# Kernel optimization log

Hardware: AMD Instinct MI355X
Metric: run time of the kernel (lower is better)

## Reference

```python
import math
import jax, jax.numpy as jnp
import numpy as np

CLUSTER_RATIO1 = 0.0625
CLUSTER_RATIO2 = 0.35
K_LAYER1 = 8
K_LAYER2 = 3


def _dpc_knn(x, cluster_num, k, key):
    """Density-peak clustering with KNN density. x: [B,N,C] -> idx_cluster [B,N]."""
    B, N, C = x.shape
    sq = jnp.sum(x * x, axis=-1)  # [B,N]
    d2 = sq[:, :, None] + sq[:, None, :] - 2.0 * jnp.einsum('bnc,bmc->bnm', x, x)
    dist = jnp.sqrt(jnp.maximum(d2, 0.0)) / jnp.sqrt(jnp.asarray(C, x.dtype))  # cdist / C**0.5
    # k nearest (smallest) distances
    neg_dn, _ = jax.lax.top_k(-dist, k)
    dist_nearest = -neg_dn  # [B,N,k]
    density = jnp.exp(-jnp.mean(dist_nearest ** 2, axis=-1))
    density = density + jax.random.uniform(key, density.shape, dtype=density.dtype) * 1e-6
    mask = (density[:, None, :] > density[:, :, None]).astype(x.dtype)  # [B,N,N]
    dist_max = jnp.max(dist.reshape(B, -1), axis=-1)[:, None, None]
    parent_dist = jnp.min(dist * mask + dist_max * (1.0 - mask), axis=-1)  # [B,N]
    score = parent_dist * density
    _, index_down = jax.lax.top_k(score, cluster_num)  # [B,cluster_num] cluster centers
    # assign each token to nearest center
    dm = jnp.take_along_axis(dist, index_down[:, :, None], axis=1)  # [B,cluster_num,N]
    idx_cluster = jnp.argmin(dm, axis=1)  # [B,N]
    bidx = jnp.arange(B)[:, None]
    idx_cluster = idx_cluster.at[bidx, index_down].set(
        jnp.broadcast_to(jnp.arange(cluster_num)[None, :], index_down.shape))
    return idx_cluster


def _merge_tokens(x, idx_cluster, cluster_num):
    """Weighted (uniform) scatter-mean of tokens into clusters. x: [B,N,C]."""
    B, N, C = x.shape
    flat = (idx_cluster + jnp.arange(B)[:, None] * cluster_num).reshape(-1)  # [B*N]
    ones = jnp.ones((B * N,), x.dtype)
    all_w = jax.ops.segment_sum(ones, flat, num_segments=B * cluster_num) + 1e-6
    norm_w = 1.0 / all_w[flat]  # token_weight == 1
    merged = jax.ops.segment_sum(x.reshape(B * N, C) * norm_w[:, None], flat,
                                 num_segments=B * cluster_num)
    return merged.reshape(B, cluster_num, C)


def _group(meta1, meta2, idx_cluster2, score_w, score_b):
    """Reorder [meta2[v]; members of cluster v from meta1] per cluster, scaled by modulation."""
    T, K1, C = meta1.shape
    K2 = meta2.shape[1]
    modu = jax.nn.softmax(meta2.mean(axis=2) @ score_w.T + score_b, axis=-1)  # [T,K2]
    # composite sort key: (cluster_id, 0 for meta2 center, 1+i for meta1 member i) -> stable grouping
    cid = jnp.concatenate([jnp.broadcast_to(jnp.arange(K2)[None, :], (T, K2)),
                           idx_cluster2], axis=1)  # [T,K2+K1]
    pos = jnp.concatenate([jnp.zeros((T, K2), jnp.int32),
                           jnp.broadcast_to(jnp.arange(1, K1 + 1, dtype=jnp.int32)[None, :], (T, K1))],
                          axis=1)
    sort_key = cid * (K1 + 2) + pos
    order = jnp.argsort(sort_key, axis=1)  # stable; keys are unique anyway
    tokens = jnp.concatenate([meta2, meta1], axis=1)  # [T,K2+K1,C]
    sorted_tokens = jnp.take_along_axis(tokens, order[:, :, None], axis=1)
    sorted_cid = jnp.take_along_axis(cid, order, axis=1)
    scale = jnp.take_along_axis(modu, sorted_cid, axis=1)  # [T,K2+K1]
    return sorted_tokens * scale[:, :, None]


def setup_inputs() -> dict:
    key = jax.random.key(0)
    k1, k2, k3 = jax.random.split(key, 3)
    T, N, C = 128, 256, 1408
    vis_embed = jax.random.normal(k1, (T, N, C), dtype=jnp.float32)
    score_w = jax.random.normal(k2, (6, 6), dtype=jnp.float32) * 0.1
    score_b = jax.random.normal(k3, (6,), dtype=jnp.float32) * 0.1
    return {"vis_embed": vis_embed, "score_w": score_w, "score_b": score_b}


def reference(vis_embed, score_w, score_b):
    T, N, C = vis_embed.shape
    cn1 = max(math.ceil(N * CLUSTER_RATIO1), 1)      # 16
    cn2 = max(math.ceil(cn1 * CLUSTER_RATIO2), 1)    # 6
    nk = jax.random.split(jax.random.key(42), 2)
    idx1 = _dpc_knn(vis_embed, cn1, K_LAYER1, nk[0])
    meta1 = _merge_tokens(vis_embed, idx1, cn1)       # [T,16,C]
    idx2 = _dpc_knn(meta1, cn2, K_LAYER2, nk[1])
    meta2 = _merge_tokens(meta1, idx2, cn2)           # [T,6,C]
    return _group(meta1, meta2, idx2, score_w, score_b)  # [T,22,C]
```

## Files before the change

kernel.cpp:

```cpp
#include <hip/hip_runtime.h>
#include <math.h>

#define T_BATCH 128
#define N_TOK   256
#define C_DIM   1408
#define CN1     16
#define KNN1    8
#define CN2     6
#define KNN2    3
#define NOUT    22
#define LS      44

typedef __attribute__((ext_vector_type(4))) short sh4;
typedef __attribute__((ext_vector_type(8))) short sh8;
typedef __attribute__((ext_vector_type(4))) float f32x4;
typedef __fp16 h2v __attribute__((ext_vector_type(2)));
typedef __fp16 h8v __attribute__((ext_vector_type(8)));

union frag_u { sh4 h[2]; sh8 v; };
union h8u { sh8 s; h8v h; };
union h2u { h2v h; unsigned u; };

__device__ inline h8v ld_frag(const short* p) {
    frag_u u;
    u.h[0] = *(const sh4*)p;
    u.h[1] = *(const sh4*)(p + 4);
    h8u o; o.s = u.v;
    return o.h;
}

__device__ inline void split2(float v0, float v1, unsigned& hip, unsigned& lop) {
    h2v h = __builtin_amdgcn_cvt_pkrtz(v0, v1);
    float r0 = v0 - (float)h[0];
    float r1 = v1 - (float)h[1];
    h2v l = __builtin_amdgcn_cvt_pkrtz(r0, r1);
    h2u uh, ul;
    uh.h = h; ul.h = l;
    hip = uh.u;
    lop = ul.u;
}

#define INS8(m, v) {                                   \
    float _x = (v);                                    \
    _Pragma("unroll")                                  \
    for (int _q = 0; _q < 8; _q++) {                   \
        float _lo = fminf(m[_q], _x);                  \
        _x = fmaxf(m[_q], _x);                         \
        m[_q] = _lo;                                   \
    }                                                  \
}

__global__ __launch_bounds__(256, 4) void gemm_dist_sym(const float* __restrict__ x,
                                                        float* __restrict__ dist) {
    const int id = blockIdx.x;
    const int r  = id & 7;
    const int q8 = id >> 3;
    const int p  = q8 % 10;
    const int tt = q8 / 10;
    const int t  = tt * 8 + r;
    const int bi = (p < 4) ? 0 : (p < 7) ? 1 : (p < 9) ? 2 : 3;
    const int bj = (p < 4) ? p : (p < 7) ? p - 3 : (p < 9) ? p - 5 : 3;
    const int i0 = bi * 64, j0 = bj * 64;
    const bool diag = (bi == bj);
    const float* X = x + (size_t)t * N_TOK * C_DIM;

    __shared__ short Ahi[64 * LS], Alo[64 * LS], Bhi[64 * LS], Blo[64 * LS];
    __shared__ float nred[512];
    __shared__ float snA[64], snB[64];

    const int tid  = threadIdx.x;
    const int wave = tid >> 6;
    const int lane = tid & 63;
    const int qr   = wave >> 1;
    const int qc   = wave & 1;
    const int srow = tid >> 2;
    const int sq   = tid & 3;
    const int fr   = lane & 15;
    const int fq   = lane >> 4;

    const short* BhiS = diag ? Ahi : Bhi;
    const short* BloS = diag ? Alo : Blo;

    f32x4 acc[2][2];
#pragma unroll
    for (int a = 0; a < 2; a++)
#pragma unroll
        for (int b = 0; b < 2; b++) acc[a][b] = (f32x4){0.f, 0.f, 0.f, 0.f};

    const float* Arow = X + (size_t)(i0 + srow) * C_DIM + sq * 8;
    const float* Brow = X + (size_t)(j0 + srow) * C_DIM + sq * 8;
    float nA = 0.f, nB = 0.f;

    float4 a0 = *(const float4*)(Arow + 0);
    float4 a1 = *(const float4*)(Arow + 4);
    float4 b0 = {0.f, 0.f, 0.f, 0.f}, b1 = {0.f, 0.f, 0.f, 0.f};
    if (!diag) {
        b0 = *(const float4*)(Brow + 0);
        b1 = *(const float4*)(Brow + 4);
    }

    for (int k0 = 0; k0 < C_DIM; k0 += 32) {
        float av[8], bv[8];
        av[0] = a0.x; av[1] = a0.y; av[2] = a0.z; av[3] = a0.w;
        av[4] = a1.x; av[5] = a1.y; av[6] = a1.z; av[7] = a1.w;
#pragma unroll
        for (int e = 0; e < 8; e++) nA += av[e] * av[e];
        unsigned ah[4], al[4], bh[4], bl[4];
#pragma unroll
        for (int q = 0; q < 4; q++) split2(av[2 * q], av[2 * q + 1], ah[q], al[q]);
        if (!diag) {
            bv[0] = b0.x; bv[1] = b0.y; bv[2] = b0.z; bv[3] = b0.w;
            bv[4] = b1.x; bv[5] = b1.y; bv[6] = b1.z; bv[7] = b1.w;
#pragma unroll
            for (int e = 0; e < 8; e++) nB += bv[e] * bv[e];
#pragma unroll
            for (int q = 0; q < 4; q++) split2(bv[2 * q], bv[2 * q + 1], bh[q], bl[q]);
        }
        __syncthreads();
        {
            unsigned* AH = (unsigned*)&Ahi[srow * LS + sq * 8];
            unsigned* AL = (unsigned*)&Alo[srow * LS + sq * 8];
#pragma unroll
            for (int q = 0; q < 4; q++) { AH[q] = ah[q]; AL[q] = al[q]; }
            if (!diag) {
                unsigned* BH = (unsigned*)&Bhi[srow * LS + sq * 8];
                unsigned* BL = (unsigned*)&Blo[srow * LS + sq * 8];
#pragma unroll
                for (int q = 0; q < 4; q++) { BH[q] = bh[q]; BL[q] = bl[q]; }
            }
        }
        __syncthreads();

        const int k1 = k0 + 32;
        if (k1 < C_DIM) {
            a0 = *(const float4*)(Arow + k1);
            a1 = *(const float4*)(Arow + k1 + 4);
            if (!diag) {
                b0 = *(const float4*)(Brow + k1);
                b1 = *(const float4*)(Brow + k1 + 4);
            }
        }

        h8v fAh[2], fAl[2], fBh[2], fBl[2];
#pragma unroll
        for (int mt = 0; mt < 2; mt++) {
            int ro = (qr * 32 + mt * 16 + fr) * LS + fq * 8;
            fAh[mt] = ld_frag(&Ahi[ro]);
            fAl[mt] = ld_frag(&Alo[ro]);
            int co = (qc * 32 + mt * 16 + fr) * LS + fq * 8;
            fBh[mt] = ld_frag(&BhiS[co]);
            fBl[mt] = ld_frag(&BloS[co]);
        }
#pragma unroll
        for (int mt = 0; mt < 2; mt++)
#pragma unroll
            for (int nt = 0; nt < 2; nt++) {
                acc[mt][nt] = __builtin_amdgcn_mfma_f32_16x16x32_f16(fAh[mt], fBh[nt], acc[mt][nt], 0, 0, 0);
                acc[mt][nt] = __builtin_amdgcn_mfma_f32_16x16x32_f16(fAh[mt], fBl[nt], acc[mt][nt], 0, 0, 0);
                acc[mt][nt] = __builtin_amdgcn_mfma_f32_16x16x32_f16(fAl[mt], fBh[nt], acc[mt][nt], 0, 0, 0);
            }
    }

    nred[tid] = nA;
    nred[256 + tid] = diag ? nA : nB;
    __syncthreads();
    if (tid < 64) {
        snA[tid] = nred[4 * tid] + nred[4 * tid + 1] + nred[4 * tid + 2] + nred[4 * tid + 3];
        snB[tid] = nred[256 + 4 * tid] + nred[256 + 4 * tid + 1]
                 + nred[256 + 4 * tid + 2] + nred[256 + 4 * tid + 3];
    }
    __syncthreads();

    const float inv_sqrtC = 1.0f / sqrtf((float)C_DIM);
    float* Dt = dist + (size_t)t * N_TOK * N_TOK;
#pragma unroll
    for (int mt = 0; mt < 2; mt++)
#pragma unroll
        for (int nt = 0; nt < 2; nt++) {
            int jl = qc * 32 + nt * 16 + fr;
            int jg = j0 + jl;
            float sqj = snB[jl];
            int il0 = qr * 32 + mt * 16 + fq * 4;
            float vv[4];
#pragma unroll
            for (int rr = 0; rr < 4; rr++) {
                int ig = i0 + il0 + rr;
                float d2 = snA[il0 + rr] + sqj - 2.0f * acc[mt][nt][rr];
                float v = (ig == jg) ? 0.0f : sqrtf(fmaxf(d2, 0.0f)) * inv_sqrtC;
                Dt[(size_t)ig * N_TOK + jg] = v;
                vv[rr] = v;
            }
            if (!diag) {
                float4 o; o.x = vv[0]; o.y = vv[1]; o.z = vv[2]; o.w = vv[3];
                *(float4*)&Dt[(size_t)jg * N_TOK + i0 + il0] = o;
            }
        }
}

__global__ __launch_bounds__(1024) void dpc1_fused(const float* __restrict__ dist,
                                                   int* __restrict__ memb,
                                                   int* __restrict__ cntg,
                                                   int* __restrict__ offg) {
    const int t    = blockIdx.x;
    const int tid  = threadIdx.x;
    const int col  = tid & 255;
    const int h    = tid >> 8;
    const int lane = tid & 63;
    const int wid  = tid >> 6;
    const float* D = dist + (size_t)t * N_TOK * N_TOK;

    __shared__ float dens_s[N_TOK];
    __shared__ float lists[KNN1][1024];
    __shared__ float red[1024];
    __shared__ float rmax16[16];
    __shared__ unsigned long long wred[16];
    __shared__ int centers[CN1];
    __shared__ int bks[N_TOK];
    __shared__ int cnt_s[CN1], off_s[CN1];

    float c0[8], c1[8];
#pragma unroll
    for (int q = 0; q < 8; q++) { c0[q] = 3.4e38f; c1[q] = 3.4e38f; }
    float mx = 0.f;
    const float* base = D + (size_t)(h * 64) * N_TOK + col;
    for (int jj = 0; jj < 64; jj += 2) {
        float d0 = base[(size_t)(jj + 0) * N_TOK];
        float d1 = base[(size_t)(jj + 1) * N_TOK];
        mx = fmaxf(mx, fmaxf(d0, d1));
        INS8(c0, d0); INS8(c1, d1);
    }
#pragma unroll
    for (int q = 0; q < 8; q++) { INS8(c0, c1[q]); }
#pragma unroll
    for (int q = 0; q < 8; q++) lists[q][tid] = c0[q];
#pragma unroll
    for (int off = 32; off > 0; off >>= 1) mx = fmaxf(mx, __shfl_xor(mx, off));
    if (lane == 0) rmax16[wid] = mx;
    __syncthreads();
    float dmax = rmax16[0];
#pragma unroll
    for (int w = 1; w < 16; w++) dmax = fmaxf(dmax, rmax16[w]);

    if (h == 0) {
#pragma unroll
        for (int s = 1; s < 4; s++)
#pragma unroll
            for (int q = 0; q < 8; q++) { float v = lists[q][col + s * 256]; INS8(c0, v); }
        float s2 = 0.f;
#pragma unroll
        for (int q = 0; q < 8; q++) s2 += c0[q] * c0[q];
        dens_s[col] = expf(-s2 / (float)KNN1);
    }
    __syncthreads();
    const float dens = dens_s[col];

    float p0 = dmax, p1 = dmax;
    const float* dsh = dens_s + h * 64;
    for (int jj = 0; jj < 64; jj += 2) {
        float d0 = base[(size_t)(jj + 0) * N_TOK];
        float d1 = base[(size_t)(jj + 1) * N_TOK];
        p0 = (dsh[jj + 0] > dens) ? fminf(p0, d0) : p0;
        p1 = (dsh[jj + 1] > dens) ? fminf(p1, d1) : p1;
    }
    red[tid] = fminf(p0, p1);
    __syncthreads();
    float score = 0.f;
    if (h == 0)
        score = fminf(fminf(red[col], red[col + 256]),
                      fminf(red[col + 512], red[col + 768])) * dens;

    unsigned long long key = 0;
    if (h == 0)
        key = ((unsigned long long)__float_as_uint(score) << 32) | (unsigned)(65535 - col);
    for (int k = 0; k < CN1; k++) {
        unsigned long long mm = key;
#pragma unroll
        for (int off = 32; off > 0; off >>= 1) {
            unsigned long long o = __shfl_xor(mm, off);
            mm = (o > mm) ? o : mm;
        }
        if (lane == 0) wred[wid] = mm;
        __syncthreads();
        unsigned long long b = wred[0];
#pragma unroll
        for (int w = 1; w < 16; w++) b = (wred[w] > b) ? wred[w] : b;
        int idx = 65535 - (int)(b & 0xFFFFull);
        if (tid == 0) centers[k] = idx;
        if (tid == idx) key = 0;
        __syncthreads();
    }

    int bk = 0;
    if (h == 0) {
        float bd = 3.4e38f;
#pragma unroll
        for (int k = 0; k < CN1; k++) {
            float d = D[(size_t)centers[k] * N_TOK + col];
            if (d < bd) { bd = d; bk = k; }
        }
#pragma unroll
        for (int k = 0; k < CN1; k++) if (col == centers[k]) bk = k;
        bks[col] = bk;
    }
    __syncthreads();
    if (tid < CN1) {
        int c = 0;
        for (int j = 0; j < N_TOK; j++) c += (bks[j] == tid);
        cnt_s[tid] = c;
    }
    __syncthreads();
    if (tid == 0) {
        int o = 0;
        for (int q = 0; q < CN1; q++) { off_s[q] = o; o += cnt_s[q]; }
    }
    __syncthreads();
    if (h == 0) {
        int rank = 0;
        for (int j = 0; j < col; j++) rank += (bks[j] == bk);
        memb[t * N_TOK + off_s[bk] + rank] = col;
    }
    if (tid < CN1) {
        cntg[t * CN1 + tid] = cnt_s[tid];
        offg[t * CN1 + tid] = off_s[tid];
    }
}

__global__ __launch_bounds__(256) void merge1_kernel(const float* __restrict__ x,
                                                     const int* __restrict__ memb,
                                                     const int* __restrict__ cntg,
                                                     const int* __restrict__ offg,
                                                     float* __restrict__ meta1) {
    const int q   = blockIdx.x;
    const int t   = blockIdx.y;
    const int tid = threadIdx.x;
    const int n    = cntg[t * CN1 + q];
    const int base = t * N_TOK + offg[t * CN1 + q];
    const int c0 = tid, c1 = tid + 256;
    const bool act1 = (c1 < C_DIM / 4);
    const float4* xb = (const float4*)(x + (size_t)t * N_TOK * C_DIM);
    const int stride4 = C_DIM / 4;

    float4 s0 = {0.f, 0.f, 0.f, 0.f};
    float4 s1 = {0.f, 0.f, 0.f, 0.f};
    int m = 0;
    for (; m + 4 <= n; m += 4) {
        int r0 = memb[base + m + 0];
        int r1 = memb[base + m + 1];
        int r2 = memb[base + m + 2];
        int r3 = memb[base + m + 3];
        float4 a0 = xb[(size_t)r0 * stride4 + c0];
        float4 a1 = xb[(size_t)r1 * stride4 + c0];
        float4 a2 = xb[(size_t)r2 * stride4 + c0];
        float4 a3 = xb[(size_t)r3 * stride4 + c0];
        s0.x += a0.x; s0.y += a0.y; s0.z += a0.z; s0.w += a0.w;
        s0.x += a1.x; s0.y += a1.y; s0.z += a1.z; s0.w += a1.w;
        s0.x += a2.x; s0.y += a2.y; s0.z += a2.z; s0.w += a2.w;
        s0.x += a3.x; s0.y += a3.y; s0.z += a3.z; s0.w += a3.w;
        if (act1) {
            float4 b0 = xb[(size_t)r0 * stride4 + c1];
            float4 b1 = xb[(size_t)r1 * stride4 + c1];
            float4 b2 = xb[(size_t)r2 * stride4 + c1];
            float4 b3 = xb[(size_t)r3 * stride4 + c1];
            s1.x += b0.x; s1.y += b0.y; s1.z += b0.z; s1.w += b0.w;
            s1.x += b1.x; s1.y += b1.y; s1.z += b1.z; s1.w += b1.w;
            s1.x += b2.x; s1.y += b2.y; s1.z += b2.z; s1.w += b2.w;
            s1.x += b3.x; s1.y += b3.y; s1.z += b3.z; s1.w += b3.w;
        }
    }
    for (; m < n; m++) {
        int r0 = memb[base + m];
        float4 a0 = xb[(size_t)r0 * stride4 + c0];
        s0.x += a0.x; s0.y += a0.y; s0.z += a0.z; s0.w += a0.w;
        if (act1) {
            float4 b0 = xb[(size_t)r0 * stride4 + c1];
            s1.x += b0.x; s1.y += b0.y; s1.z += b0.z; s1.w += b0.w;
        }
    }
    float w = 1.0f / ((float)n + 1e-6f);
    float4* mr = (float4*)(meta1 + ((size_t)t * CN1 + q) * C_DIM);
    float4 o0; o0.x = s0.x * w; o0.y = s0.y * w; o0.z = s0.z * w; o0.w = s0.w * w;
    mr[c0] = o0;
    if (act1) {
        float4 o1; o1.x = s1.x * w; o1.y = s1.y * w; o1.z = s1.z * w; o1.w = s1.w * w;
        mr[c1] = o1;
    }
}

__global__ __launch_bounds__(1024) void layer2_kernel(const float* __restrict__ meta1,
                                                      const float* __restrict__ score_w,
                                                      const float* __restrict__ score_b,
                                                      float* __restrict__ out) {
    const int t   = blockIdx.x & 127;
    const int bh  = blockIdx.x >> 7;
    const int tid = threadIdx.x;
    const float* M = meta1 + (size_t)t * CN1 * C_DIM;

    __shared__ float buf[CN1][132];
    __shared__ float d2s[CN1][CN1];
    __shared__ float m2[CN2][C_DIM];
    __shared__ float dens[CN1], scor[CN1], nrm[CN1], rmx[CN1];
    __shared__ int   centers[CN2], idx2s[CN1], cnt2[CN2];
    __shared__ float modu[CN2], msum[CN2];
    __shared__ int   srcRow[NOUT], cidArr[NOUT];
    __shared__ float dmax_sh;

    const int ti = (tid < 256) ? (tid >> 4) : 0;
    const int tj = tid & 15;

    float acc = 0.f;
    for (int c0 = 0; c0 < C_DIM; c0 += 128) {
        for (int e = tid; e < CN1 * 128; e += 1024) {
            int r = e >> 7, c = e & 127;
            buf[r][c] = M[(size_t)r * C_DIM + c0 + c];
        }
        __syncthreads();
        if (tid < 256) {
#pragma unroll
            for (int cc = 0; cc < 128; cc += 4) {
                float4 a = *(const float4*)&buf[ti][cc];
                float4 b = *(const float4*)&buf[tj][cc];
                acc += a.x * b.x + a.y * b.y + a.z * b.z + a.w * b.w;
            }
        }
        __syncthreads();
    }
    if (tid < 256 && ti == tj) nrm[ti] = acc;
    __syncthreads();

    const float inv_sqrtC = 1.0f / sqrtf((float)C_DIM);
    if (tid < 256) {
        float d2 = nrm[ti] + nrm[tj] - 2.f * acc;
        d2s[ti][tj] = sqrtf(fmaxf(d2, 0.f)) * inv_sqrtC;
    }
    __syncthreads();

    if (tid < CN1) {
        float m0 = 3.4e38f, m1 = 3.4e38f, m2v = 3.4e38f, mx = 0.f;
        for (int j = 0; j < CN1; j++) {
            float d = d2s[tid][j];
            mx = fmaxf(mx, d);
            if (d < m2v) {
                m2v = d;
                if (m2v < m1) { float tmp = m2v; m2v = m1; m1 = tmp; }
                if (m1 < m0)  { float tmp = m1;  m1 = m0;  m0 = tmp; }
            }
        }
        dens[tid] = expf(-(m0 * m0 + m1 * m1 + m2v * m2v) / (float)KNN2);
        rmx[tid] = mx;
    }
    __syncthreads();
    if (tid == 0) {
        float g = 0.f;
        for (int j = 0; j < CN1; j++) g = fmaxf(g, rmx[j]);
        dmax_sh = g;
    }
    __syncthreads();

    if (tid < CN1) {
        float di = dens[tid];
        float pd = dmax_sh;
        for (int j = 0; j < CN1; j++)
            if (dens[j] > di) pd = fminf(pd, d2s[tid][j]);
        scor[tid] = pd * di;
    }
    __syncthreads();

    if (tid == 0) {
        for (int k = 0; k < CN2; k++) {
            float best = -3.4e38f; int bi = 0;
            for (int j = 0; j < CN1; j++)
                if (scor[j] > best) { best = scor[j]; bi = j; }
            centers[k] = bi;
            scor[bi] = -3.4e38f;
        }
    }
    __syncthreads();

    if (tid < CN1) {
        float bd = 3.4e38f; int bk = 0;
#pragma unroll
        for (int k = 0; k < CN2; k++) {
            float d = d2s[centers[k]][tid];
            if (d < bd) { bd = d; bk = k; }
        }
#pragma unroll
        for (int k = 0; k < CN2; k++) if (tid == centers[k]) bk = k;
        idx2s[tid] = bk;
    }
    __syncthreads();

    if (tid == 0) {
        for (int v = 0; v < CN2; v++) cnt2[v] = 0;
        for (int i = 0; i < CN1; i++) cnt2[idx2s[i]]++;
        int slot = 0;
        for (int v = 0; v < CN2; v++) {
            srcRow[slot] = CN1 + v; cidArr[slot] = v; slot++;
            for (int i = 0; i < CN1; i++)
                if (idx2s[i] == v) { srcRow[slot] = i; cidArr[slot] = v; slot++; }
        }
        for (int v = 0; v < CN2; v++) msum[v] = 0.f;
    }
    __syncthreads();

    float ls[CN2] = {0.f, 0.f, 0.f, 0.f, 0.f, 0.f};
    for (int ch = tid; ch < C_DIM; ch += 1024) {
        float a6[CN2] = {0.f, 0.f, 0.f, 0.f, 0.f, 0.f};
        for (int r = 0; r < CN1; r++) {
            float v = M[(size_t)r * C_DIM + ch];
            int c = idx2s[r];
#pragma unroll
            for (int q = 0; q < CN2; q++) a6[q] += (c == q) ? v : 0.f;
        }
#pragma unroll
        for (int q = 0; q < CN2; q++) {
            float mv = a6[q] / ((float)cnt2[q] + 1e-6f);
            m2[q][ch] = mv;
            ls[q] += mv;
        }
    }
#pragma unroll
    for (int q = 0; q < CN2; q++) atomicAdd(&msum[q], ls[q]);
    __syncthreads();

    if (tid == 0) {
        float mean[CN2], lg[CN2];
        for (int v = 0; v < CN2; v++) mean[v] = msum[v] / (float)C_DIM;
        float mxl = -3.4e38f;
        for (int u = 0; u < CN2; u++) {
            float s = score_b[u];
            for (int v = 0; v < CN2; v++) s += mean[v] * score_w[u * CN2 + v];
            lg[u] = s;
            mxl = fmaxf(mxl, s);
        }
        float den = 0.f;
        for (int u = 0; u < CN2; u++) { lg[u] = expf(lg[u] - mxl); den += lg[u]; }
        for (int u = 0; u < CN2; u++) modu[u] = lg[u] / den;
    }
    __syncthreads();

    const int chLo = bh * (C_DIM / 2);
    const int chHi = chLo + (C_DIM / 2);
    float* ob = out + (size_t)t * NOUT * C_DIM;
    for (int ch = chLo + tid; ch < chHi; ch += 1024) {
#pragma unroll
        for (int s = 0; s < NOUT; s++) {
            int r = srcRow[s];
            float v = (r < CN1) ? M[(size_t)r * C_DIM + ch] : m2[r - CN1][ch];
            ob[(size_t)s * C_DIM + ch] = v * modu[cidArr[s]];
        }
    }
}

extern "C" void kernel_launch(void* const* d_in, const int* in_sizes, int n_in,
                              void* d_out, int out_size, void* d_ws, size_t ws_size,
                              hipStream_t stream) {
    const float* x  = (const float*)d_in[0];
    const float* sw = (const float*)d_in[1];
    const float* sb = (const float*)d_in[2];
    float* out = (float*)d_out;

    float* ws     = (float*)d_ws;
    float* dist   = ws;
    float* meta1  = dist + (size_t)T_BATCH * N_TOK * N_TOK;
    int*   memb   = (int*)(meta1 + (size_t)T_BATCH * CN1 * C_DIM);
    int*   cntg   = memb + (size_t)T_BATCH * N_TOK;
    int*   offg   = cntg + T_BATCH * CN1;

    gemm_dist_sym<<<1280, 256, 0, stream>>>(x, dist);
    dpc1_fused<<<T_BATCH, 1024, 0, stream>>>(dist, memb, cntg, offg);
    merge1_kernel<<<dim3(CN1, T_BATCH), 256, 0, stream>>>(x, memb, cntg, offg, meta1);
    layer2_kernel<<<2 * T_BATCH, 1024, 0, stream>>>(meta1, sw, sb, out);
}
```

Measured before the change: 413.0 us.

## Load MFMA fragments directly from global memory, bypassing shared-memory staging

The distance GEMM kernel now has each lane load its own fp32 operand fragments from global memory, split them into fp16 hi/lo pairs in registers, and feed them straight to MFMA. Shared-memory tiles and the two barriers per k-step are gone, and row norms are reduced with wave shuffles. The cost is redundant global loads and conversions, since each A row is loaded by both column waves and each B row by both row waves. Diagonal tiles also no longer reuse the A operand for B.

```diff
diff --git a/kernel.cpp b/kernel.cpp
--- a/kernel.cpp
+++ b/kernel.cpp
@@ -9,7 +9,6 @@
 #define CN2     6
 #define KNN2    3
 #define NOUT    22
-#define LS      44
 
 typedef __attribute__((ext_vector_type(4))) short sh4;
 typedef __attribute__((ext_vector_type(8))) short sh8;
@@ -17,17 +16,8 @@
 typedef __fp16 h2v __attribute__((ext_vector_type(2)));
 typedef __fp16 h8v __attribute__((ext_vector_type(8)));
 
-union frag_u { sh4 h[2]; sh8 v; };
-union h8u { sh8 s; h8v h; };
 union h2u { h2v h; unsigned u; };
-
-__device__ inline h8v ld_frag(const short* p) {
-    frag_u u;
-    u.h[0] = *(const sh4*)p;
-    u.h[1] = *(const sh4*)(p + 4);
-    h8u o; o.s = u.v;
-    return o.h;
-}
+union h8pack { unsigned u[4]; h8v h; };
 
 __device__ inline void split2(float v0, float v1, unsigned& hip, unsigned& lop) {
     h2v h = __builtin_amdgcn_cvt_pkrtz(v0, v1);
@@ -40,6 +30,18 @@
     lop = ul.u;
 }
 
+__device__ inline void cvt8(const float4 u, const float4 v, h8v& hi, h8v& lo, float& nrm) {
+    nrm += u.x * u.x + u.y * u.y + u.z * u.z + u.w * u.w
+         + v.x * v.x + v.y * v.y + v.z * v.z + v.w * v.w;
+    h8pack ph, pl;
+    split2(u.x, u.y, ph.u[0], pl.u[0]);
+    split2(u.z, u.w, ph.u[1], pl.u[1]);
+    split2(v.x, v.y, ph.u[2], pl.u[2]);
+    split2(v.z, v.w, ph.u[3], pl.u[3]);
+    hi = ph.h;
+    lo = pl.h;
+}
+
 #define INS8(m, v) {                                   \
     float _x = (v);                                    \
     _Pragma("unroll")                                  \
@@ -50,7 +52,7 @@
     }                                                  \
 }
 
-__global__ __launch_bounds__(256, 4) void gemm_dist_sym(const float* __restrict__ x,
+__global__ __launch_bounds__(256, 4) void gemm_dist_reg(const float* __restrict__ x,
                                                         float* __restrict__ dist) {
     const int id = blockIdx.x;
     const int r  = id & 7;
@@ -64,8 +66,6 @@
     const bool diag = (bi == bj);
     const float* X = x + (size_t)t * N_TOK * C_DIM;
 
-    __shared__ short Ahi[64 * LS], Alo[64 * LS], Bhi[64 * LS], Blo[64 * LS];
-    __shared__ float nred[512];
     __shared__ float snA[64], snB[64];
 
     const int tid  = threadIdx.x;
@@ -73,84 +73,49 @@
     const int lane = tid & 63;
     const int qr   = wave >> 1;
     const int qc   = wave & 1;
-    const int srow = tid >> 2;
-    const int sq   = tid & 3;
     const int fr   = lane & 15;
     const int fq   = lane >> 4;
 
-    const short* BhiS = diag ? Ahi : Bhi;
-    const short* BloS = diag ? Alo : Blo;
-
     f32x4 acc[2][2];
 #pragma unroll
     for (int a = 0; a < 2; a++)
 #pragma unroll
         for (int b = 0; b < 2; b++) acc[a][b] = (f32x4){0.f, 0.f, 0.f, 0.f};
 
-    const float* Arow = X + (size_t)(i0 + srow) * C_DIM + sq * 8;
-    const float* Brow = X + (size_t)(j0 + srow) * C_DIM + sq * 8;
-    float nA = 0.f, nB = 0.f;
-
-    float4 a0 = *(const float4*)(Arow + 0);
-    float4 a1 = *(const float4*)(Arow + 4);
-    float4 b0 = {0.f, 0.f, 0.f, 0.f}, b1 = {0.f, 0.f, 0.f, 0.f};
-    if (!diag) {
-        b0 = *(const float4*)(Brow + 0);
-        b1 = *(const float4*)(Brow + 4);
-    }
+    const float* pA0 = X + (size_t)(i0 + qr * 32 + fr) * C_DIM + fq * 8;
+    const float* pA1 = pA0 + (size_t)16 * C_DIM;
+    const float* pB0 = X + (size_t)(j0 + qc * 32 + fr) * C_DIM + fq * 8;
+    const float* pB1 = pB0 + (size_t)16 * C_DIM;
+    float nA0 = 0.f, nA1 = 0.f, nB0 = 0.f, nB1 = 0.f;
+
+    float4 a00 = *(const float4*)(pA0);
+    float4 a01 = *(const float4*)(pA0 + 4);
+    float4 a10 = *(const float4*)(pA1);
+    float4 a11 = *(const float4*)(pA1 + 4);
+    float4 b00 = *(const float4*)(pB0);
+    float4 b01 = *(const float4*)(pB0 + 4);
+    float4 b10 = *(const float4*)(pB1);
+    float4 b11 = *(const float4*)(pB1 + 4);
 
     for (int k0 = 0; k0 < C_DIM; k0 += 32) {
-        float av[8], bv[8];
-        av[0] = a0.x; av[1] = a0.y; av[2] = a0.z; av[3] = a0.w;
-        av[4] = a1.x; av[5] = a1.y; av[6] = a1.z; av[7] = a1.w;
-#pragma unroll
-        for (int e = 0; e < 8; e++) nA += av[e] * av[e];
-        unsigned ah[4], al[4], bh[4], bl[4];
-#pragma unroll
-        for (int q = 0; q < 4; q++) split2(av[2 * q], av[2 * q + 1], ah[q], al[q]);
-        if (!diag) {
-            bv[0] = b0.x; bv[1] = b0.y; bv[2] = b0.z; bv[3] = b0.w;
-            bv[4] = b1.x; bv[5] = b1.y; bv[6] = b1.z; bv[7] = b1.w;
-#pragma unroll
-            for (int e = 0; e < 8; e++) nB += bv[e] * bv[e];
-#pragma unroll
-            for (int q = 0; q < 4; q++) split2(bv[2 * q], bv[2 * q + 1], bh[q], bl[q]);
-        }
-        __syncthreads();
-        {
-            unsigned* AH = (unsigned*)&Ahi[srow * LS + sq * 8];
-            unsigned* AL = (unsigned*)&Alo[srow * LS + sq * 8];
-#pragma unroll
-            for (int q = 0; q < 4; q++) { AH[q] = ah[q]; AL[q] = al[q]; }
-            if (!diag) {
-                unsigned* BH = (unsigned*)&Bhi[srow * LS + sq * 8];
-                unsigned* BL = (unsigned*)&Blo[srow * LS + sq * 8];
-#pragma unroll
-                for (int q = 0; q < 4; q++) { BH[q] = bh[q]; BL[q] = bl[q]; }
-            }
-        }
-        __syncthreads();
+        h8v fAh[2], fAl[2], fBh[2], fBl[2];
+        cvt8(a00, a01, fAh[0], fAl[0], nA0);
+        cvt8(a10, a11, fAh[1], fAl[1], nA1);
+        cvt8(b00, b01, fBh[0], fBl[0], nB0);
+        cvt8(b10, b11, fBh[1], fBl[1], nB1);
 
         const int k1 = k0 + 32;
         if (k1 < C_DIM) {
-            a0 = *(const float4*)(Arow + k1);
-            a1 = *(const float4*)(Arow + k1 + 4);
-            if (!diag) {
-                b0 = *(const float4*)(Brow + k1);
-                b1 = *(const float4*)(Brow + k1 + 4);
-            }
-        }
-
-        h8v fAh[2], fAl[2], fBh[2], fBl[2];
-#pragma unroll
-        for (int mt = 0; mt < 2; mt++) {
-            int ro = (qr * 32 + mt * 16 + fr) * LS + fq * 8;
-            fAh[mt] = ld_frag(&Ahi[ro]);
-            fAl[mt] = ld_frag(&Alo[ro]);
-            int co = (qc * 32 + mt * 16 + fr) * LS + fq * 8;
-            fBh[mt] = ld_frag(&BhiS[co]);
-            fBl[mt] = ld_frag(&BloS[co]);
-        }
+            a00 = *(const float4*)(pA0 + k1);
+            a01 = *(const float4*)(pA0 + k1 + 4);
+            a10 = *(const float4*)(pA1 + k1);
+            a11 = *(const float4*)(pA1 + k1 + 4);
+            b00 = *(const float4*)(pB0 + k1);
+            b01 = *(const float4*)(pB0 + k1 + 4);
+            b10 = *(const float4*)(pB1 + k1);
+            b11 = *(const float4*)(pB1 + k1 + 4);
+        }
+
 #pragma unroll
         for (int mt = 0; mt < 2; mt++)
 #pragma unroll
@@ -161,13 +126,17 @@
             }
     }
 
-    nred[tid] = nA;
-    nred[256 + tid] = diag ? nA : nB;
-    __syncthreads();
-    if (tid < 64) {
-        snA[tid] = nred[4 * tid] + nred[4 * tid + 1] + nred[4 * tid + 2] + nred[4 * tid + 3];
-        snB[tid] = nred[256 + 4 * tid] + nred[256 + 4 * tid + 1]
-                 + nred[256 + 4 * tid + 2] + nred[256 + 4 * tid + 3];
+    nA0 += __shfl_xor(nA0, 16); nA0 += __shfl_xor(nA0, 32);
+    nA1 += __shfl_xor(nA1, 16); nA1 += __shfl_xor(nA1, 32);
+    nB0 += __shfl_xor(nB0, 16); nB0 += __shfl_xor(nB0, 32);
+    nB1 += __shfl_xor(nB1, 16); nB1 += __shfl_xor(nB1, 32);
+    if (fq == 0 && qc == 0) {
+        snA[qr * 32 + fr]      = nA0;
+        snA[qr * 32 + 16 + fr] = nA1;
+    }
+    if (fq == 0 && qr == 0) {
+        snB[qc * 32 + fr]      = nB0;
+        snB[qc * 32 + 16 + fr] = nB1;
     }
     __syncthreads();
 
@@ -566,7 +535,7 @@
     int*   cntg   = memb + (size_t)T_BATCH * N_TOK;
     int*   offg   = cntg + T_BATCH * CN1;
 
-    gemm_dist_sym<<<1280, 256, 0, stream>>>(x, dist);
+    gemm_dist_reg<<<1280, 256, 0, stream>>>(x, dist);
     dpc1_fused<<<T_BATCH, 1024, 0, stream>>>(dist, memb, cntg, offg);
     merge1_kernel<<<dim3(CN1, T_BATCH), 256, 0, stream>>>(x, memb, cntg, offg, meta1);
     layer2_kernel<<<2 * T_BATCH, 1024, 0, stream>>>(meta1, sw, sb, out);
```

New measurement: 567.3 us. +37.4%, slower.
